# Performance work log

Hardware: AMD Instinct MI355X
Metric: run time of the kernel (lower is better)

The kernel has to match this reference:

```python
import jax, jax.numpy as jnp
import numpy as np

N_NODES = 100000
N_EDGES = 1600000
D_IN = 128
D_HID = 128
N_CLS = 16
N_GRAPHS = 64


def setup_inputs() -> dict:
    key = jax.random.key(0)
    ks = jax.random.split(key, 12)
    h = jax.random.normal(ks[0], (N_NODES, D_IN), dtype=jnp.float32)
    src = jax.random.randint(ks[1], (N_EDGES,), 0, N_NODES, dtype=jnp.int32)
    dst = jax.random.randint(ks[2], (N_EDGES,), 0, N_NODES, dtype=jnp.int32)
    graph_ids = jnp.sort(jax.random.randint(ks[3], (N_NODES,), 0, N_GRAPHS, dtype=jnp.int32))
    s = 1.0 / np.sqrt(D_IN)
    W1_self = jax.random.uniform(ks[4], (D_IN, D_HID), jnp.float32, -s, s)
    W1_neigh = jax.random.uniform(ks[5], (D_IN, D_HID), jnp.float32, -s, s)
    b1 = jnp.zeros((D_HID,), jnp.float32)
    s2 = 1.0 / np.sqrt(D_HID)
    W2_self = jax.random.uniform(ks[6], (D_HID, D_HID), jnp.float32, -s2, s2)
    W2_neigh = jax.random.uniform(ks[7], (D_HID, D_HID), jnp.float32, -s2, s2)
    b2 = jnp.zeros((D_HID,), jnp.float32)
    Wc = jax.random.uniform(ks[8], (D_HID, N_CLS), jnp.float32, -s2, s2)
    bc = jnp.zeros((N_CLS,), jnp.float32)
    return {"h": h, "src": src, "dst": dst, "graph_ids": graph_ids, "num_graphs": N_GRAPHS,
            "W1_self": W1_self, "W1_neigh": W1_neigh, "b1": b1,
            "W2_self": W2_self, "W2_neigh": W2_neigh, "b2": b2,
            "Wc": Wc, "bc": bc}


def _sage_conv(h, src, dst, W_self, W_neigh, b):
    # DGL SAGEConv 'mean': out = fc_self(h) + fc_neigh(mean of in-neighbor feats) + bias
    n = h.shape[0]
    msg = jnp.take(h, src, axis=0)                               # [E, d] gather
    agg = jax.ops.segment_sum(msg, dst, num_segments=n)          # [N, d] scatter-add
    deg = jax.ops.segment_sum(jnp.ones((src.shape[0],), h.dtype), dst, num_segments=n)
    neigh = agg / jnp.maximum(deg, 1.0)[:, None]                 # mean, zero-degree safe
    return h @ W_self + neigh @ W_neigh + b


def reference(h, src, dst, graph_ids, num_graphs,
              W1_self, W1_neigh, b1, W2_self, W2_neigh, b2, Wc, bc):
    x = jax.nn.relu(_sage_conv(h, src, dst, W1_self, W1_neigh, b1))
    x = _sage_conv(x, src, dst, W2_self, W2_neigh, b2)
    # dgl.mean_nodes: per-graph mean over node features
    gsum = jax.ops.segment_sum(x, graph_ids, num_segments=num_graphs)    # [G, d]
    gcnt = jax.ops.segment_sum(jnp.ones((x.shape[0],), x.dtype), graph_ids, num_segments=num_graphs)
    hg = gsum / jnp.maximum(gcnt, 1.0)[:, None]
    return hg @ Wc + bc                                                  # [G, num_classes]
```

## Files before the change

### kernel.cpp

```cpp
#include <hip/hip_runtime.h>

#define D        128
#define N_GRAPHS 64
#define N_CLS    16
#define LDA      40
#define SLOTS    48
#define CAP      8192

typedef unsigned int   uint;
typedef unsigned short ushort;
typedef __attribute__((ext_vector_type(8))) short short8;
typedef __attribute__((ext_vector_type(4))) float f32x4;

__device__ inline ushort f2b(float f) {
    uint u = __float_as_uint(f);
    u += 0x7fffu + ((u >> 16) & 1u);
    return (ushort)(u >> 16);
}

__device__ __forceinline__ int swz2i(int row, int col) {
    return row * 256 + (col ^ (((row ^ (row >> 3)) & 7) << 3));
}


__global__ __launch_bounds__(256) void k_boot(
    const float* __restrict__ h, ushort* __restrict__ fb,
    const float* __restrict__ Ws, const float* __restrict__ Wn,
    ushort* __restrict__ wT,
    const int* __restrict__ gid, int* __restrict__ gstart,
    const int* __restrict__ src, const int* __restrict__ dst,
    int* __restrict__ bcount, uint* __restrict__ ebuf,
    int E, int NB, int N, int t4) {
    __shared__ int hist[512], base[512], lcur[512];
    int bb = blockIdx.x;
    int t  = threadIdx.x;

    if (bb < 256) {
        int per = (E + 255) / 256;
        int e0 = bb * per;
        int e1 = min(e0 + per, E);
        for (int i = t; i < NB; i += 256) { hist[i] = 0; lcur[i] = 0; }
        __syncthreads();
        for (int e = e0 + t; e < e1; e += 256) atomicAdd(&hist[dst[e] >> 8], 1);
        __syncthreads();
        for (int i = t; i < NB; i += 256)
            base[i] = hist[i] ? atomicAdd(&bcount[i], hist[i]) : 0;
        __syncthreads();
        for (int e = e0 + t; e < e1; e += 256) {
            int dd = dst[e];
            int b = dd >> 8;
            int off = atomicAdd(&lcur[b], 1);
            int pos = base[b] + off;
            if (pos < CAP)
                ebuf[(size_t)b * CAP + pos] = ((uint)src[e] << 8) | (uint)(dd & 255);
        }
    } else if (bb < 384) {
        int i = (bb - 256) * 256 + t;
        int c = i >> 8, k = i & 255;
        float v = (k < 128) ? Ws[k * 128 + c] : Wn[(k - 128) * 128 + c];
        wT[c * 256 + k] = f2b(v);
    } else if (bb == 384) {
        int g = t;
        if (g <= N_GRAPHS) {
            int lo = 0, hi = N;
            while (lo < hi) {
                int mid = (lo + hi) >> 1;
                if (gid[mid] < g) lo = mid + 1; else hi = mid;
            }
            gstart[g] = lo;
        }
    } else {
        int i = (bb - 385) * 256 + t;
        if (i < t4) {
            float4 v = ((const float4*)h)[i];
            ushort4 o;
            o.x = f2b(v.x); o.y = f2b(v.y); o.z = f2b(v.z); o.w = f2b(v.w);
            ((ushort4*)fb)[i] = o;
        }
    }
}


__global__ __launch_bounds__(1024) void k_bucket(
    const uint* __restrict__ ebuf, const int* __restrict__ bcount,
    int* __restrict__ csrf, int* __restrict__ deg, float* __restrict__ invdeg,
    int N) {
    __shared__ int ldeg[256];
    __shared__ int lcsr[256 * SLOTS];
    int b = blockIdx.x, t = threadIdx.x;
    if (t < 256) ldeg[t] = 0;
    __syncthreads();
    int cnt = bcount[b];
    if (cnt > CAP) cnt = CAP;
    const uint* __restrict__ eb = ebuf + (size_t)b * CAP;
    for (int i = t; i < cnt; i += 1024) {
        uint r = eb[i];
        int dl = r & 255;
        int sl = atomicAdd(&ldeg[dl], 1);
        if (sl < SLOTS) lcsr[dl * SLOTS + sl] = (int)(r >> 8);
    }
    __syncthreads();
    int n0 = b << 8;
    int lim = (N - n0) * SLOTS;
    if (lim > 256 * SLOTS) lim = 256 * SLOTS;
    for (int i = t; i < lim; i += 1024)
        csrf[(size_t)n0 * SLOTS + i] = lcsr[i];
    if (t < 256 && n0 + t < N) {
        int d = ldeg[t];
        deg[n0 + t] = d;
        invdeg[n0 + t] = 1.0f / (float)(d > 1 ? d : 1);
    }
}


__global__ __launch_bounds__(256) void k_aggb(
    const ushort* __restrict__ fb, const int* __restrict__ deg,
    const int* __restrict__ csrf, const float* __restrict__ invdeg,
    ushort* __restrict__ outb, int N) {
    int lane = threadIdx.x & 63;
    int n = blockIdx.x * 4 + (threadIdx.x >> 6);
    if (n >= N) return;
    int d = deg[n];
    if (d > SLOTS) d = SLOTS;
    const int* __restrict__ lst = csrf + (size_t)n * SLOTS;
    int ej = lane >> 4;
    int cg = lane & 15;

    float acc[8];
#pragma unroll
    for (int i = 0; i < 8; i++) acc[i] = 0.f;

    int e = ej;
    for (; e + 4 < d; e += 8) {
        int s0 = lst[e];
        int s1 = lst[e + 4];
        uint4 v0 = *(const uint4*)(fb + (size_t)s0 * D + cg * 8);
        uint4 v1 = *(const uint4*)(fb + (size_t)s1 * D + cg * 8);
        acc[0] += __uint_as_float(v0.x << 16);
        acc[1] += __uint_as_float(v0.x & 0xffff0000u);
        acc[2] += __uint_as_float(v0.y << 16);
        acc[3] += __uint_as_float(v0.y & 0xffff0000u);
        acc[4] += __uint_as_float(v0.z << 16);
        acc[5] += __uint_as_float(v0.z & 0xffff0000u);
        acc[6] += __uint_as_float(v0.w << 16);
        acc[7] += __uint_as_float(v0.w & 0xffff0000u);
        acc[0] += __uint_as_float(v1.x << 16);
        acc[1] += __uint_as_float(v1.x & 0xffff0000u);
        acc[2] += __uint_as_float(v1.y << 16);
        acc[3] += __uint_as_float(v1.y & 0xffff0000u);
        acc[4] += __uint_as_float(v1.z << 16);
        acc[5] += __uint_as_float(v1.z & 0xffff0000u);
        acc[6] += __uint_as_float(v1.w << 16);
        acc[7] += __uint_as_float(v1.w & 0xffff0000u);
    }
    for (; e < d; e += 4) {
        int s = lst[e];
        uint4 v = *(const uint4*)(fb + (size_t)s * D + cg * 8);
        acc[0] += __uint_as_float(v.x << 16);
        acc[1] += __uint_as_float(v.x & 0xffff0000u);
        acc[2] += __uint_as_float(v.y << 16);
        acc[3] += __uint_as_float(v.y & 0xffff0000u);
        acc[4] += __uint_as_float(v.z << 16);
        acc[5] += __uint_as_float(v.z & 0xffff0000u);
        acc[6] += __uint_as_float(v.w << 16);
        acc[7] += __uint_as_float(v.w & 0xffff0000u);
    }
#pragma unroll
    for (int i = 0; i < 8; i++) {
        acc[i] += __shfl_xor(acc[i], 16);
        acc[i] += __shfl_xor(acc[i], 32);
    }
    if (ej == 0) {
        float id = invdeg[n];
        uint4 o;
        o.x = (uint)f2b(acc[0] * id) | ((uint)f2b(acc[1] * id) << 16);
        o.y = (uint)f2b(acc[2] * id) | ((uint)f2b(acc[3] * id) << 16);
        o.z = (uint)f2b(acc[4] * id) | ((uint)f2b(acc[5] * id) << 16);
        o.w = (uint)f2b(acc[6] * id) | ((uint)f2b(acc[7] * id) << 16);
        *(uint4*)(outb + (size_t)n * D + cg * 8) = o;
    }
}


__global__ __launch_bounds__(256, 2) void k_mmp2(
    const ushort* __restrict__ hb, const ushort* __restrict__ nbb,
    const ushort* __restrict__ wT, const float* __restrict__ b,
    ushort* __restrict__ x1b, int N, int MMB,
    const int* __restrict__ src, const int* __restrict__ dst,
    const int* __restrict__ gid, const int* __restrict__ deg,
    int* __restrict__ bcount2, uint* __restrict__ ebuf2, int E, int NB) {
    __shared__ __align__(16) ushort As[128 * LDA];
    __shared__ __align__(16) ushort Bs[128 * LDA];
    __shared__ int hist[512], base[512], lcur[512];

    if (blockIdx.x >= MMB) {
        int bb = blockIdx.x - MMB;
        int t = threadIdx.x;
        int per = (E + 255) / 256;
        int e0 = bb * per;
        int e1 = min(e0 + per, E);
        for (int i = t; i < NB; i += 256) { hist[i] = 0; lcur[i] = 0; }
        __syncthreads();
        for (int e = e0 + t; e < e1; e += 256) atomicAdd(&hist[src[e] >> 8], 1);
        __syncthreads();
        for (int i = t; i < NB; i += 256)
            base[i] = hist[i] ? atomicAdd(&bcount2[i], hist[i]) : 0;
        __syncthreads();
        for (int e = e0 + t; e < e1; e += 256) {
            int ss = src[e];
            int dd = dst[e];
            int bk = ss >> 8;
            int off = atomicAdd(&lcur[bk], 1);
            int pos = base[bk] + off;
            if (pos < CAP) {
                int g  = gid[dd];
                int dc = deg[dd]; if (dc > 127) dc = 127;
                ebuf2[(size_t)bk * CAP + pos] =
                    (uint)(ss & 255) | ((uint)g << 8) | ((uint)dc << 14);
            }
        }
        return;
    }

    int t    = threadIdx.x;
    int w    = t >> 6;
    int lane = t & 63;
    int m    = lane & 15;
    int quad = lane >> 4;
    int n0   = blockIdx.x * 128;

    f32x4 acc[2][8];
#pragma unroll
    for (int rt = 0; rt < 2; rt++)
#pragma unroll
        for (int ct = 0; ct < 8; ct++) acc[rt][ct] = (f32x4){0.f, 0.f, 0.f, 0.f};

#pragma unroll 1
    for (int kc = 0; kc < 8; kc++) {
        int k0 = kc * 32;
        const ushort* __restrict__ A = (k0 < 128) ? hb : nbb;
        int ka = k0 & 127;
        __syncthreads();
#pragma unroll
        for (int i = 0; i < 2; i++) {
            int linear = i * 256 + t;
            int row = linear >> 2;
            int q   = linear & 3;
            int nn = n0 + row;
            uint4 v = make_uint4(0u, 0u, 0u, 0u);
            if (nn < N) v = *(const uint4*)(A + (size_t)nn * D + ka + q * 8);
            *(uint4*)(&As[row * LDA + q * 8]) = v;
        }
#pragma unroll
        for (int i = 0; i < 2; i++) {
            int linear = i * 256 + t;
            int col = linear >> 2;
            int q   = linear & 3;
            uint4 v = *(const uint4*)(wT + (size_t)col * 256 + k0 + q * 8);
            *(uint4*)(&Bs[col * LDA + q * 8]) = v;
        }
        __syncthreads();
        short8 af[2], bf[8];
#pragma unroll
        for (int rt = 0; rt < 2; rt++)
            af[rt] = *(const short8*)(&As[(w * 32 + rt * 16 + m) * LDA + quad * 8]);
#pragma unroll
        for (int ct = 0; ct < 8; ct++)
            bf[ct] = *(const short8*)(&Bs[(ct * 16 + m) * LDA + quad * 8]);
#pragma unroll
        for (int rt = 0; rt < 2; rt++)
#pragma unroll
            for (int ct = 0; ct < 8; ct++)
                acc[rt][ct] = __builtin_amdgcn_mfma_f32_16x16x32_bf16(
                    af[rt], bf[ct], acc[rt][ct], 0, 0, 0);
    }
#pragma unroll
    for (int ct = 0; ct < 8; ct++) {
        float bias = b[ct * 16 + m];
#pragma unroll
        for (int rt = 0; rt < 2; rt++) {
#pragma unroll
            for (int r = 0; r < 4; r++) {
                int n = n0 + w * 32 + rt * 16 + quad * 4 + r;
                if (n < N)
                    x1b[(size_t)n * D + ct * 16 + m] =
                        f2b(fmaxf(acc[rt][ct][r] + bias, 0.f));
            }
        }
    }
}


__global__ __launch_bounds__(1024, 4) void k_wg(
    const uint* __restrict__ ebuf2, const int* __restrict__ bcount2,
    const ushort* __restrict__ x1b, const int* __restrict__ gstart,
    float* __restrict__ S1, float* __restrict__ P, int N, int WSB) {
    __shared__ __align__(16) char smem[131072];

    if (blockIdx.x >= WSB) {
        int b2 = blockIdx.x - WSB;
        int g  = b2 >> 1;
        int ch = b2 & 1;
        int r0 = gstart[g], r1 = gstart[g + 1];
        int len = r1 - r0;
        if (len <= 0) return;
        int L = (len + 1) >> 1;
        int a = r0 + ch * L;
        int bnd = min(a + L, r1);
        if (a >= bnd) return;
        int rp = threadIdx.x >> 6;
        int cp = threadIdx.x & 63;
        float ax = 0.f, ay = 0.f;
        const uint* __restrict__ M = (const uint*)x1b;
        for (int n = a + rp; n < bnd; n += 16) {
            uint v = M[(size_t)n * 64 + cp];
            ax += __uint_as_float(v << 16);
            ay += __uint_as_float(v & 0xffff0000u);
        }
        atomicAdd(&S1[g * D + cp * 2], ax);
        atomicAdd(&S1[g * D + cp * 2 + 1], ay);
        return;
    }

    float*  lwcT = (float*)smem;
    ushort* lxT  = (ushort*)smem;
    ushort* lwcb = (ushort*)(smem + 65536);
    ushort* lwlo = (ushort*)(smem + 98304);

    int b = blockIdx.x, t = threadIdx.x;
    int n0 = b << 8;

    for (int i = t; i < 16384; i += 1024) lwcT[i] = 0.f;
    __syncthreads();

    int cnt = bcount2[b];
    if (cnt > CAP) cnt = CAP;
    const uint* __restrict__ eb = ebuf2 + (size_t)b * CAP;
    for (int i = t; i < cnt; i += 1024) {
        uint r = eb[i];
        int sl = (int)(r & 255u);
        int g  = (int)((r >> 8) & 63u);
        int dc = (int)((r >> 14) & 127u);
        float id = 1.0f / (float)(dc > 1 ? dc : 1);
        atomicAdd(&lwcT[g * 256 + sl], id);
    }
    __syncthreads();

    for (int i = t; i < 16384; i += 1024) {
        int g = i >> 8, sl = i & 255;
        float v = lwcT[i];
        ushort hi = f2b(v);
        float fhi = __uint_as_float((uint)hi << 16);
        ushort lo = f2b(v - fhi);
        int si = swz2i(g, sl);
        lwcb[si] = hi;
        lwlo[si] = lo;
    }
    __syncthreads();

    const uint4* __restrict__ x4 = (const uint4*)x1b;
#pragma unroll 1
    for (int it = 0; it < 4; ++it) {
        int l = it * 1024 + t;
        int n = l >> 4, q = l & 15;
        uint4 v = make_uint4(0u, 0u, 0u, 0u);
        int nn = n0 + n;
        if (nn < N) v = x4[(size_t)nn * 16 + q];
        int d0 = q * 8;
        lxT[swz2i(d0 + 0, n)] = (ushort)(v.x & 0xffffu);
        lxT[swz2i(d0 + 1, n)] = (ushort)(v.x >> 16);
        lxT[swz2i(d0 + 2, n)] = (ushort)(v.y & 0xffffu);
        lxT[swz2i(d0 + 3, n)] = (ushort)(v.y >> 16);
        lxT[swz2i(d0 + 4, n)] = (ushort)(v.z & 0xffffu);
        lxT[swz2i(d0 + 5, n)] = (ushort)(v.z >> 16);
        lxT[swz2i(d0 + 6, n)] = (ushort)(v.w & 0xffffu);
        lxT[swz2i(d0 + 7, n)] = (ushort)(v.w >> 16);
    }
    __syncthreads();

    int wv = t >> 6, lane = t & 63, m = lane & 15, quad = lane >> 4;
    int s  = wv & 3;
    int hs = wv >> 2;
    f32x4 acc[2];
    acc[0] = (f32x4){0.f, 0.f, 0.f, 0.f};
    acc[1] = (f32x4){0.f, 0.f, 0.f, 0.f};

#pragma unroll 1
    for (int k8 = 0; k8 < 8; ++k8) {
        int kc = k8 * 32 + quad * 8;
        int ar = s * 16 + m;
        short8 ahi = *(const short8*)&lwcb[swz2i(ar, kc)];
        short8 alo = *(const short8*)&lwlo[swz2i(ar, kc)];
#pragma unroll
        for (int d2 = 0; d2 < 2; ++d2) {
            short8 bfr = *(const short8*)&lxT[swz2i(hs * 32 + d2 * 16 + m, kc)];
            acc[d2] = __builtin_amdgcn_mfma_f32_16x16x32_bf16(alo, bfr, acc[d2], 0, 0, 0);
            acc[d2] = __builtin_amdgcn_mfma_f32_16x16x32_bf16(ahi, bfr, acc[d2], 0, 0, 0);
        }
    }
    float* __restrict__ Pb = P + (size_t)b * 8192;
#pragma unroll
    for (int d2 = 0; d2 < 2; ++d2) {
#pragma unroll
        for (int r = 0; r < 4; ++r) {
            int g = s * 16 + quad * 4 + r;
            Pb[g * 128 + hs * 32 + d2 * 16 + m] = acc[d2][r];
        }
    }
}


__global__ __launch_bounds__(256) void k_final(
    const float* __restrict__ S1, const float* __restrict__ P, int NBLK,
    const int* __restrict__ gstart, const float* __restrict__ W2s,
    const float* __restrict__ W2n, const float* __restrict__ b2,
    const float* __restrict__ Wc, const float* __restrict__ bc,
    float* __restrict__ out) {
    __shared__ float s1[D], s2[2][D], hg[D];
    int g = blockIdx.x, t = threadIdx.x;
    int c = t & 127, hh = t >> 7;
    const float* __restrict__ Pg = P + (size_t)g * 128 + c;
    float a0 = 0.f, a1 = 0.f, a2 = 0.f, a3 = 0.f;
    int bb = hh;
    for (; bb + 6 < NBLK; bb += 8) {
        a0 += Pg[(size_t)bb * 8192];
        a1 += Pg[(size_t)(bb + 2) * 8192];
        a2 += Pg[(size_t)(bb + 4) * 8192];
        a3 += Pg[(size_t)(bb + 6) * 8192];
    }
    for (; bb < NBLK; bb += 2) a0 += Pg[(size_t)bb * 8192];
    s2[hh][c] = a0 + a1 + a2 + a3;
    if (hh == 0) s1[c] = S1[g * D + c];
    __syncthreads();
    if (t < 128) s2[0][c] += s2[1][c];
    __syncthreads();
    if (t < 128) {
        float acc = 0.f;
#pragma unroll 8
        for (int k = 0; k < D; k++) {
            acc = fmaf(s1[k], W2s[k * D + c], acc);
            acc = fmaf(s2[0][k], W2n[k * D + c], acc);
        }
        int cnt = gstart[g + 1] - gstart[g];
        hg[c] = (cnt > 0) ? (acc / (float)cnt + b2[c]) : 0.f;
    }
    __syncthreads();
    if (t < N_CLS) {
        float o = bc[t];
        for (int k = 0; k < D; k++) o = fmaf(hg[k], Wc[k * N_CLS + t], o);
        out[g * N_CLS + t] = o;
    }
}


extern "C" void kernel_launch(void* const* d_in, const int* in_sizes, int n_in,
                              void* d_out, int out_size, void* d_ws, size_t ws_size,
                              hipStream_t stream) {
    const float* h   = (const float*)d_in[0];
    const int*   src = (const int*)d_in[1];
    const int*   dst = (const int*)d_in[2];
    const int*   gid = (const int*)d_in[3];
    const float* W1s = (const float*)d_in[5];
    const float* W1n = (const float*)d_in[6];
    const float* b1  = (const float*)d_in[7];
    const float* W2s = (const float*)d_in[8];
    const float* W2n = (const float*)d_in[9];
    const float* b2  = (const float*)d_in[10];
    const float* Wc  = (const float*)d_in[11];
    const float* bc  = (const float*)d_in[12];
    float* out = (float*)d_out;

    const int N = in_sizes[0] / D;
    const int E = in_sizes[1];
    const int NB = (N + 255) >> 8;

    char* w = (char*)d_ws;
    size_t off = 0;
    auto alloc = [&](size_t elems) -> void* {
        void* p = w + off;
        off += elems * 4;
        return p;
    };
    float* S1      = (float*)alloc((size_t)N_GRAPHS * D);
    int*   bcount  = (int*)alloc(512);
    int*   bcount2 = (int*)alloc(512);
    size_t zero_bytes = off;
    int*   deg    = (int*)alloc(N);
    float* invdeg = (float*)alloc(N);
    int*   gstart = (int*)alloc(128);
    int*   csrf   = (int*)alloc((size_t)N * SLOTS);
    ushort* fb    = (ushort*)alloc((size_t)N * 64);
    ushort* nbb   = (ushort*)alloc((size_t)N * 64);
    ushort* x1b   = (ushort*)alloc((size_t)N * 64);
    ushort* wT    = (ushort*)alloc(16384);
    uint*  ebuf  = (uint*)nbb;
    uint*  ebuf2 = (uint*)csrf;
    float* P     = (float*)fb;
    (void)ws_size;

    hipMemsetAsync(d_ws, 0, zero_bytes, stream);

    int t4 = N * 32;
    int CB = (t4 + 255) / 256;
    int MMB = (N + 127) / 128;

    k_boot<<<256 + 128 + 1 + CB, 256, 0, stream>>>(
        h, fb, W1s, W1n, wT, gid, gstart, src, dst, bcount, ebuf, E, NB, N, t4);
    k_bucket<<<NB, 1024, 0, stream>>>(ebuf, bcount, csrf, deg, invdeg, N);
    k_aggb<<<(N + 3) / 4, 256, 0, stream>>>(fb, deg, csrf, invdeg, nbb, N);
    k_mmp2<<<MMB + 256, 256, 0, stream>>>(
        fb, nbb, wT, b1, x1b, N, MMB, src, dst, gid, deg, bcount2, ebuf2, E, NB);
    k_wg<<<NB + 128, 1024, 0, stream>>>(
        ebuf2, bcount2, x1b, gstart, S1, P, N, NB);
    k_final<<<N_GRAPHS, 256, 0, stream>>>(
        S1, P, NB, gstart, W2s, W2n, b2, Wc, bc, out);
}
```

Before: 334.4 us.

## Move second edge partition into aggregation kernel using dedicated buffer

Moves the second-layer edge bucketing pass out of the first-layer matmul kernel and into the extra blocks of the aggregation kernel. When the workspace is large enough it gets its own buffer instead of aliasing the CSR array, so it can run alongside aggregation, which still reads the CSR. The matmul kernel becomes a pure GEMM without the extra shared histogram arrays. If the workspace is too small, a separate partition kernel runs after aggregation as a fallback.

```diff
diff --git a/kernel.cpp b/kernel.cpp
--- a/kernel.cpp
+++ b/kernel.cpp
@@ -113,10 +113,44 @@
 }
 
 
-__global__ __launch_bounds__(256) void k_aggb(
+__global__ __launch_bounds__(256) void k_agp(
     const ushort* __restrict__ fb, const int* __restrict__ deg,
     const int* __restrict__ csrf, const float* __restrict__ invdeg,
-    ushort* __restrict__ outb, int N) {
+    ushort* __restrict__ outb, int N, int AB,
+    const int* __restrict__ src, const int* __restrict__ dst,
+    const int* __restrict__ gid,
+    int* __restrict__ bcount2, uint* __restrict__ ebuf2, int E, int NB) {
+    __shared__ int hist[512], base[512], lcur[512];
+
+    if (blockIdx.x >= AB) {
+        int bb = blockIdx.x - AB;
+        int t = threadIdx.x;
+        int per = (E + 255) / 256;
+        int e0 = bb * per;
+        int e1 = min(e0 + per, E);
+        for (int i = t; i < NB; i += 256) { hist[i] = 0; lcur[i] = 0; }
+        __syncthreads();
+        for (int e = e0 + t; e < e1; e += 256) atomicAdd(&hist[src[e] >> 8], 1);
+        __syncthreads();
+        for (int i = t; i < NB; i += 256)
+            base[i] = hist[i] ? atomicAdd(&bcount2[i], hist[i]) : 0;
+        __syncthreads();
+        for (int e = e0 + t; e < e1; e += 256) {
+            int ss = src[e];
+            int dd = dst[e];
+            int bk = ss >> 8;
+            int off = atomicAdd(&lcur[bk], 1);
+            int pos = base[bk] + off;
+            if (pos < CAP) {
+                int g  = gid[dd];
+                int dc = deg[dd]; if (dc > 127) dc = 127;
+                ebuf2[(size_t)bk * CAP + pos] =
+                    (uint)(ss & 255) | ((uint)g << 8) | ((uint)dc << 14);
+            }
+        }
+        return;
+    }
+
     int lane = threadIdx.x & 63;
     int n = blockIdx.x * 4 + (threadIdx.x >> 6);
     if (n >= N) return;
@@ -181,47 +215,44 @@
     }
 }
 
-
-__global__ __launch_bounds__(256, 2) void k_mmp2(
-    const ushort* __restrict__ hb, const ushort* __restrict__ nbb,
-    const ushort* __restrict__ wT, const float* __restrict__ b,
-    ushort* __restrict__ x1b, int N, int MMB,
+__global__ __launch_bounds__(256) void k_part2s(
     const int* __restrict__ src, const int* __restrict__ dst,
     const int* __restrict__ gid, const int* __restrict__ deg,
     int* __restrict__ bcount2, uint* __restrict__ ebuf2, int E, int NB) {
+    __shared__ int hist[512], base[512], lcur[512];
+    int t = threadIdx.x;
+    int per = (E + 255) / 256;
+    int e0 = blockIdx.x * per;
+    int e1 = min(e0 + per, E);
+    for (int i = t; i < NB; i += 256) { hist[i] = 0; lcur[i] = 0; }
+    __syncthreads();
+    for (int e = e0 + t; e < e1; e += 256) atomicAdd(&hist[src[e] >> 8], 1);
+    __syncthreads();
+    for (int i = t; i < NB; i += 256)
+        base[i] = hist[i] ? atomicAdd(&bcount2[i], hist[i]) : 0;
+    __syncthreads();
+    for (int e = e0 + t; e < e1; e += 256) {
+        int ss = src[e];
+        int dd = dst[e];
+        int bk = ss >> 8;
+        int off = atomicAdd(&lcur[bk], 1);
+        int pos = base[bk] + off;
+        if (pos < CAP) {
+            int g  = gid[dd];
+            int dc = deg[dd]; if (dc > 127) dc = 127;
+            ebuf2[(size_t)bk * CAP + pos] =
+                (uint)(ss & 255) | ((uint)g << 8) | ((uint)dc << 14);
+        }
+    }
+}
+
+
+__global__ __launch_bounds__(256, 2) void k_mm1m(
+    const ushort* __restrict__ hb, const ushort* __restrict__ nbb,
+    const ushort* __restrict__ wT, const float* __restrict__ b,
+    ushort* __restrict__ x1b, int N) {
     __shared__ __align__(16) ushort As[128 * LDA];
     __shared__ __align__(16) ushort Bs[128 * LDA];
-    __shared__ int hist[512], base[512], lcur[512];
-
-    if (blockIdx.x >= MMB) {
-        int bb = blockIdx.x - MMB;
-        int t = threadIdx.x;
-        int per = (E + 255) / 256;
-        int e0 = bb * per;
-        int e1 = min(e0 + per, E);
-        for (int i = t; i < NB; i += 256) { hist[i] = 0; lcur[i] = 0; }
-        __syncthreads();
-        for (int e = e0 + t; e < e1; e += 256) atomicAdd(&hist[src[e] >> 8], 1);
-        __syncthreads();
-        for (int i = t; i < NB; i += 256)
-            base[i] = hist[i] ? atomicAdd(&bcount2[i], hist[i]) : 0;
-        __syncthreads();
-        for (int e = e0 + t; e < e1; e += 256) {
-            int ss = src[e];
-            int dd = dst[e];
-            int bk = ss >> 8;
-            int off = atomicAdd(&lcur[bk], 1);
-            int pos = base[bk] + off;
-            if (pos < CAP) {
-                int g  = gid[dd];
-                int dc = deg[dd]; if (dc > 127) dc = 127;
-                ebuf2[(size_t)bk * CAP + pos] =
-                    (uint)(ss & 255) | ((uint)g << 8) | ((uint)dc << 14);
-            }
-        }
-        return;
-    }
-
     int t    = threadIdx.x;
     int w    = t >> 6;
     int lane = t & 63;
@@ -493,23 +524,29 @@
     ushort* nbb   = (ushort*)alloc((size_t)N * 64);
     ushort* x1b   = (ushort*)alloc((size_t)N * 64);
     ushort* wT    = (ushort*)alloc(16384);
-    uint*  ebuf  = (uint*)nbb;
-    uint*  ebuf2 = (uint*)csrf;
-    float* P     = (float*)fb;
-    (void)ws_size;
+    uint*  ebuf = (uint*)nbb;
+    float* P    = (float*)fb;
+
+    size_t ebuf2_units = (size_t)NB * CAP;
+    bool dedicated = (off + ebuf2_units * 4) <= ws_size;
+    uint* ebuf2 = dedicated ? (uint*)alloc(ebuf2_units) : (uint*)csrf;
 
     hipMemsetAsync(d_ws, 0, zero_bytes, stream);
 
     int t4 = N * 32;
     int CB = (t4 + 255) / 256;
     int MMB = (N + 127) / 128;
+    int AB  = (N + 3) / 4;
 
     k_boot<<<256 + 128 + 1 + CB, 256, 0, stream>>>(
         h, fb, W1s, W1n, wT, gid, gstart, src, dst, bcount, ebuf, E, NB, N, t4);
     k_bucket<<<NB, 1024, 0, stream>>>(ebuf, bcount, csrf, deg, invdeg, N);
-    k_aggb<<<(N + 3) / 4, 256, 0, stream>>>(fb, deg, csrf, invdeg, nbb, N);
-    k_mmp2<<<MMB + 256, 256, 0, stream>>>(
-        fb, nbb, wT, b1, x1b, N, MMB, src, dst, gid, deg, bcount2, ebuf2, E, NB);
+    k_agp<<<AB + (dedicated ? 256 : 0), 256, 0, stream>>>(
+        fb, deg, csrf, invdeg, nbb, N, AB,
+        src, dst, gid, bcount2, ebuf2, E, NB);
+    if (!dedicated)
+        k_part2s<<<256, 256, 0, stream>>>(src, dst, gid, deg, bcount2, ebuf2, E, NB);
+    k_mm1m<<<MMB, 256, 0, stream>>>(fb, nbb, wT, b1, x1b, N);
     k_wg<<<NB + 128, 1024, 0, stream>>>(
         ebuf2, bcount2, x1b, gstart, S1, P, N, NB);
     k_final<<<N_GRAPHS, 256, 0, stream>>>(
```

Measured after the change: 353.7 us. 1.06x slower.
